# Performance work log

Hardware: AMD Instinct MI355X
Metric: run time of the kernel (lower is better)

Reference implementation:

```python
import jax, jax.numpy as jnp
import numpy as np

N_BLOCKS = 12   # grid rows == cols
D = 256         # per-block feature size (small -> memory-bound)
BATCH = 8192    # samples per block

# Deterministic block-sparse pattern: block (i, j) is active iff (i - j) % 3 == 0.
_mask = np.array([[(i - j) % 3 == 0 for j in range(N_BLOCKS)] for i in range(N_BLOCKS)])
_I, _J = np.nonzero(_mask)  # 48 active blocks
N_ACTIVE = _I.shape[0]


def setup_inputs() -> dict:
    key = jax.random.key(0)
    k1, k2, k3 = jax.random.split(key, 3)
    X = jax.random.normal(k1, (N_BLOCKS, BATCH, D), dtype=jnp.float32)
    # One Linear(D, D) per active block: weight [K, D_in, D_out], bias [K, D_out]
    W = jax.random.normal(k2, (N_ACTIVE, D, D), dtype=jnp.float32) / np.sqrt(D).astype(np.float32)
    b = jax.random.normal(k3, (N_ACTIVE, D), dtype=jnp.float32) * 0.01
    i_idx = jnp.asarray(_I, dtype=jnp.int32)  # output-row index of each active block
    j_idx = jnpim if False else jnp.asarray(_J, dtype=jnp.int32)  # input-col index of each active block
    return {"X": X, "W": W, "b": b, "i_idx": i_idx, "j_idx": j_idx}


def reference(X, W, b, i_idx, j_idx):
    # Gather the input block feeding each active sub-module: [K, BATCH, D]
    Xg = X[j_idx]
    # Apply each block's Linear in one batched contraction: [K, BATCH, D]
    h = jnp.einsum('kbi,kio->kbo', Xg, W) + b[:, None, :]
    # Sum block outputs into their output rows (the '+' combiner / safe_sum):
    # rows with no active block get an all-zero output, matching the zero-vector semantics.
    y = jax.ops.segment_sum(h, i_idx, num_segments=N_BLOCKS)  # [N_BLOCKS, BATCH, D]
    return y
```

## Files before the change

### kernel.cpp

```cpp
#include <hip/hip_runtime.h>

#define N_BLOCKS 12
#define D 256
#define BATCH 8192

typedef __attribute__((ext_vector_type(8))) short bf16x8;
typedef __attribute__((ext_vector_type(4))) float f32x4;

__device__ __forceinline__ unsigned short f2bf(float f) {
  unsigned int u = __float_as_uint(f);
  u += 0x7fffu + ((u >> 16) & 1u);
  return (unsigned short)(u >> 16);
}

__device__ __forceinline__ void gld16(const unsigned short* g, unsigned short* l) {
  __builtin_amdgcn_global_load_lds(
      (const __attribute__((address_space(1))) unsigned int*)g,
      (__attribute__((address_space(3))) unsigned int*)l,
      16, 0, 0);
}

__global__ void cvt_x(const float* __restrict__ X, unsigned short* __restrict__ Xb) {
  const long long t = (long long)blockIdx.x * 256 + threadIdx.x;
  const long long base = t * 8;
  const float4 v0 = *(const float4*)(X + base);
  const float4 v1 = *(const float4*)(X + base + 4);
  uint4 r;
  r.x = (unsigned)f2bf(v0.x) | ((unsigned)f2bf(v0.y) << 16);
  r.y = (unsigned)f2bf(v0.z) | ((unsigned)f2bf(v0.w) << 16);
  r.z = (unsigned)f2bf(v1.x) | ((unsigned)f2bf(v1.y) << 16);
  r.w = (unsigned)f2bf(v1.z) | ((unsigned)f2bf(v1.w) << 16);
  *(uint4*)(Xb + base) = r;
}

__global__ void cvt_w(const float* __restrict__ W, unsigned short* __restrict__ Wt) {
  __shared__ unsigned short tile[32][33];
  const int k  = blockIdx.x >> 6;
  const int t  = blockIdx.x & 63;
  const int ti = t >> 3;
  const int tj = t & 7;
  const float* Wk = W + (long long)k * D * D;
  unsigned short* Wtk = Wt + (long long)k * D * D;
  const int lx = threadIdx.x & 31, ly = threadIdx.x >> 5;
  #pragma unroll
  for (int r = 0; r < 4; ++r) {
    const int i = ti * 32 + ly + r * 8;
    const int o = tj * 32 + lx;
    tile[ly + r * 8][lx] = f2bf(Wk[i * D + o]);
  }
  __syncthreads();
  #pragma unroll
  for (int r = 0; r < 4; ++r) {
    const int o = tj * 32 + ly + r * 8;
    const int i = ti * 32 + lx;
    Wtk[o * D + i] = tile[lx][ly + r * 8];
  }
}

__launch_bounds__(256)
__global__ void bs_gemm(const unsigned short* __restrict__ Xb,
                        const unsigned short* __restrict__ Wt,
                        const float* __restrict__ bias,
                        const int* __restrict__ i_idx,
                        const int* __restrict__ j_idx,
                        int nact,
                        float* __restrict__ Y) {
  __shared__ unsigned short sA[128 * 32];
  __shared__ unsigned short sB[128 * 32];

  const int bid = blockIdx.x;
  const int x   = bid & 7;
  const int r   = bid >> 3;
  const int i   = r >> 4;
  const int rem = r & 15;
  const int bm  = x * 8 + (rem >> 1);
  const int bn  = rem & 1;

  int ks[8], js[8], nk = 0;
  for (int k = 0; k < nact; ++k)
    if (i_idx[k] == i && nk < 8) { ks[nk] = k; js[nk] = j_idx[k]; ++nk; }

  const int tid  = threadIdx.x;
  const int wave = tid >> 6;
  const int lane = tid & 63;
  const int wr   = wave >> 1, wc = wave & 1;

  const int g_off = (tid >> 2) * D + (tid & 3) * 8;
  unsigned short* lA0 = sA + tid * 8;
  unsigned short* lA1 = sA + 2048 + tid * 8;
  unsigned short* lB0 = sB + tid * 8;
  unsigned short* lB1 = sB + 2048 + tid * 8;

  const int q      = lane >> 4;
  const int frag_k = q * 8;
  const int a_row  = wr * 64 + (lane & 15);
  const int b_row  = wc * 64 + (lane & 15);

  f32x4 acc[4][4] = {};

  for (int t = 0; t < nk; ++t) {
    const unsigned short* Ab = Xb + ((long long)js[t] * BATCH + bm * 128) * D + g_off;
    const unsigned short* Bb = Wt + ((long long)ks[t] * D + bn * 128) * D + g_off;
    #pragma unroll
    for (int d0 = 0; d0 < D; d0 += 32) {
      gld16(Ab + d0, lA0);
      gld16(Ab + 64 * D + d0, lA1);
      gld16(Bb + d0, lB0);
      gld16(Bb + 64 * D + d0, lB1);
      __syncthreads();

      bf16x8 aF[4], bF[4];
      #pragma unroll
      for (int mt = 0; mt < 4; ++mt)
        aF[mt] = *(const bf16x8*)(sA + (a_row + mt * 16) * 32 + frag_k);
      #pragma unroll
      for (int nt = 0; nt < 4; ++nt)
        bF[nt] = *(const bf16x8*)(sB + (b_row + nt * 16) * 32 + frag_k);
      #pragma unroll
      for (int mt = 0; mt < 4; ++mt)
        #pragma unroll
        for (int nt = 0; nt < 4; ++nt)
          acc[mt][nt] = __builtin_amdgcn_mfma_f32_16x16x32_bf16(
              aF[mt], bF[nt], acc[mt][nt], 0, 0, 0);
      __syncthreads();
    }
  }

  float* Yb = Y + (long long)i * BATCH * D;
  const int m0 = bm * 128 + wr * 64 + (q * 4);
  const int n0 = bn * 128 + wc * 64 + (lane & 15);
  float bsum[4];
  #pragma unroll
  for (int nt = 0; nt < 4; ++nt) {
    float s = 0.f;
    for (int t = 0; t < nk; ++t) s += bias[ks[t] * D + n0 + nt * 16];
    bsum[nt] = s;
  }
  #pragma unroll
  for (int nt = 0; nt < 4; ++nt) {
    #pragma unroll
    for (int mt = 0; mt < 4; ++mt)
      #pragma unroll
      for (int r2 = 0; r2 < 4; ++r2)
        Yb[(long long)(m0 + mt * 16 + r2) * D + (n0 + nt * 16)] = acc[mt][nt][r2] + bsum[nt];
  }
}

extern "C" void kernel_launch(void* const* d_in, const int* in_sizes, int n_in,
                              void* d_out, int out_size, void* d_ws, size_t ws_size,
                              hipStream_t stream) {
  const float* X = (const float*)d_in[0];
  const float* W = (const float*)d_in[1];
  const float* b = (const float*)d_in[2];
  const int* i_idx = (const int*)d_in[3];
  const int* j_idx = (const int*)d_in[4];
  float* Y = (float*)d_out;
  const int nact = in_sizes[3];

  unsigned short* Xb = (unsigned short*)d_ws;
  unsigned short* Wt = (unsigned short*)((char*)d_ws + (size_t)N_BLOCKS * BATCH * D * 2);

  cvt_x<<<(N_BLOCKS * BATCH * D) / (256 * 8), 256, 0, stream>>>(X, Xb);
  cvt_w<<<nact * 64, 256, 0, stream>>>(W, Wt);
  bs_gemm<<<N_BLOCKS * 64 * 2, 256, 0, stream>>>(Xb, Wt, b, i_idx, j_idx, nact, Y);
}
```

Measured before the change: 261.1 us.

## Triple-buffer LDS pipeline with swizzle and 256x128 tiles in block-sparse GEMM

Restructures the GEMM main loop into a flattened 32-step pipeline across all active blocks, using three LDS stages, prefetching two stages ahead, and a single barrier per step. The tile grows to 256x128 with 512 threads. The LDS layout gets an XOR swizzle to avoid bank conflicts, and blocks are remapped across XCDs for locality. It also caps the number of active blocks per row at 4 with hardcoded registers, which is a correctness risk if more than 4 blocks are active, and it assumes exactly 4 blocks per row by hardcoding 32 steps.

```diff
diff --git a/kernel.cpp b/kernel.cpp
--- a/kernel.cpp
+++ b/kernel.cpp
@@ -57,7 +57,7 @@
   }
 }
 
-__launch_bounds__(256)
+__launch_bounds__(512, 4)
 __global__ void bs_gemm(const unsigned short* __restrict__ Xb,
                         const unsigned short* __restrict__ Wt,
                         const float* __restrict__ bias,
@@ -65,85 +65,130 @@
                         const int* __restrict__ j_idx,
                         int nact,
                         float* __restrict__ Y) {
-  __shared__ unsigned short sA[128 * 32];
-  __shared__ unsigned short sB[128 * 32];
-
-  const int bid = blockIdx.x;
-  const int x   = bid & 7;
-  const int r   = bid >> 3;
-  const int i   = r >> 4;
-  const int rem = r & 15;
-  const int bm  = x * 8 + (rem >> 1);
-  const int bn  = rem & 1;
-
-  int ks[8], js[8], nk = 0;
-  for (int k = 0; k < nact; ++k)
-    if (i_idx[k] == i && nk < 8) { ks[nk] = k; js[nk] = j_idx[k]; ++nk; }
+  __shared__ unsigned short lds[3 * 12288];
+
+  const int bid   = blockIdx.x;
+  const int xcd   = bid & 7;
+  const int local = bid >> 3;
+  const int pp    = local >> 5;
+  const int bm    = local & 31;
+  const int p     = xcd * 3 + pp;
+  const int i     = p >> 1;
+  const int bn    = p & 1;
+
+  int ks0 = 0, ks1 = 0, ks2 = 0, ks3 = 0, js0 = 0, js1 = 0, js2 = 0, js3 = 0, nk = 0;
+  for (int k = 0; k < nact; ++k) {
+    if (i_idx[k] == i) {
+      const int j = j_idx[k];
+      if      (nk == 0) { ks0 = k; js0 = j; }
+      else if (nk == 1) { ks1 = k; js1 = j; }
+      else if (nk == 2) { ks2 = k; js2 = j; }
+      else              { ks3 = k; js3 = j; }
+      ++nk;
+    }
+  }
+#define JS(t) ((t) == 0 ? js0 : (t) == 1 ? js1 : (t) == 2 ? js2 : js3)
+#define KS(t) ((t) == 0 ? ks0 : (t) == 1 ? ks1 : (t) == 2 ? ks2 : ks3)
 
   const int tid  = threadIdx.x;
   const int wave = tid >> 6;
   const int lane = tid & 63;
-  const int wr   = wave >> 1, wc = wave & 1;
-
-  const int g_off = (tid >> 2) * D + (tid & 3) * 8;
-  unsigned short* lA0 = sA + tid * 8;
-  unsigned short* lA1 = sA + 2048 + tid * 8;
-  unsigned short* lB0 = sB + tid * 8;
-  unsigned short* lB1 = sB + 2048 + tid * 8;
-
-  const int q      = lane >> 4;
-  const int frag_k = q * 8;
-  const int a_row  = wr * 64 + (lane & 15);
-  const int b_row  = wc * 64 + (lane & 15);
+  const int wm   = wave >> 1;
+  const int wn   = wave & 1;
+  const int q    = lane >> 4;
+  const int l15  = lane & 15;
+
+  const int srow = tid >> 2;
+  const int sc   = (tid & 3) ^ (srow & 3);
+  const long long sA0 = (long long)srow * D + sc * 8;
+  const long long sA1 = (long long)(srow + 128) * D + sc * 8;
+  const long long sB0 = (long long)srow * D + sc * 8;
+  const int dA0 = tid * 8;
+  const int dA1 = 4096 + tid * 8;
+  const int dB0 = 8192 + tid * 8;
+
+  const int sw  = (q ^ (l15 & 3)) << 4;
+  const int aR0 = (wm * 64 +  0 + l15) * 64 + sw;
+  const int aR1 = (wm * 64 + 16 + l15) * 64 + sw;
+  const int aR2 = (wm * 64 + 32 + l15) * 64 + sw;
+  const int aR3 = (wm * 64 + 48 + l15) * 64 + sw;
+  const int bR0 = 16384 + (wn * 64 +  0 + l15) * 64 + sw;
+  const int bR1 = 16384 + (wn * 64 + 16 + l15) * 64 + sw;
+  const int bR2 = 16384 + (wn * 64 + 32 + l15) * 64 + sw;
+  const int bR3 = 16384 + (wn * 64 + 48 + l15) * 64 + sw;
+
+  auto STAGE = [&](int st) {
+    const int t  = st >> 3;
+    const int kk = st & 7;
+    unsigned short* sl = lds + (st % 3) * 12288;
+    const unsigned short* As =
+        Xb + ((long long)JS(t) * BATCH + bm * 256) * D + kk * 32;
+    const unsigned short* Bs =
+        Wt + ((long long)KS(t) * D + bn * 128) * D + kk * 32;
+    gld16(As + sA0, sl + dA0);
+    gld16(As + sA1, sl + dA1);
+    gld16(Bs + sB0, sl + dB0);
+  };
 
   f32x4 acc[4][4] = {};
 
-  for (int t = 0; t < nk; ++t) {
-    const unsigned short* Ab = Xb + ((long long)js[t] * BATCH + bm * 128) * D + g_off;
-    const unsigned short* Bb = Wt + ((long long)ks[t] * D + bn * 128) * D + g_off;
+  STAGE(0);
+  STAGE(1);
+
+  #pragma unroll
+  for (int kt = 0; kt < 32; ++kt) {
+    if (kt == 31) asm volatile("s_waitcnt vmcnt(0)" ::: "memory");
+    else          asm volatile("s_waitcnt vmcnt(3)" ::: "memory");
+    __builtin_amdgcn_s_barrier();
+    __builtin_amdgcn_sched_barrier(0);
+
+    const char* sb = (const char*)(lds + (kt % 3) * 12288);
+    bf16x8 aF[4], bF[4];
+    aF[0] = *(const bf16x8*)(sb + aR0);
+    aF[1] = *(const bf16x8*)(sb + aR1);
+    aF[2] = *(const bf16x8*)(sb + aR2);
+    aF[3] = *(const bf16x8*)(sb + aR3);
+    bF[0] = *(const bf16x8*)(sb + bR0);
+    bF[1] = *(const bf16x8*)(sb + bR1);
+    bF[2] = *(const bf16x8*)(sb + bR2);
+    bF[3] = *(const bf16x8*)(sb + bR3);
+
+    if (kt < 30) STAGE(kt + 2);
+
+    asm volatile("s_waitcnt lgkmcnt(0)" ::: "memory");
+    __builtin_amdgcn_sched_barrier(0);
+
+    __builtin_amdgcn_s_setprio(1);
     #pragma unroll
-    for (int d0 = 0; d0 < D; d0 += 32) {
-      gld16(Ab + d0, lA0);
-      gld16(Ab + 64 * D + d0, lA1);
-      gld16(Bb + d0, lB0);
-      gld16(Bb + 64 * D + d0, lB1);
-      __syncthreads();
-
-      bf16x8 aF[4], bF[4];
+    for (int mf = 0; mf < 4; ++mf)
       #pragma unroll
-      for (int mt = 0; mt < 4; ++mt)
-        aF[mt] = *(const bf16x8*)(sA + (a_row + mt * 16) * 32 + frag_k);
-      #pragma unroll
-      for (int nt = 0; nt < 4; ++nt)
-        bF[nt] = *(const bf16x8*)(sB + (b_row + nt * 16) * 32 + frag_k);
-      #pragma unroll
-      for (int mt = 0; mt < 4; ++mt)
-        #pragma unroll
-        for (int nt = 0; nt < 4; ++nt)
-          acc[mt][nt] = __builtin_amdgcn_mfma_f32_16x16x32_bf16(
-              aF[mt], bF[nt], acc[mt][nt], 0, 0, 0);
-      __syncthreads();
-    }
+      for (int nf = 0; nf < 4; ++nf)
+        acc[mf][nf] = __builtin_amdgcn_mfma_f32_16x16x32_bf16(
+            aF[mf], bF[nf], acc[mf][nf], 0, 0, 0);
+    __builtin_amdgcn_s_setprio(0);
   }
 
   float* Yb = Y + (long long)i * BATCH * D;
-  const int m0 = bm * 128 + wr * 64 + (q * 4);
-  const int n0 = bn * 128 + wc * 64 + (lane & 15);
+  const int m0 = bm * 256 + wm * 64 + q * 4;
+  const int n0 = bn * 128 + wn * 64 + l15;
   float bsum[4];
   #pragma unroll
-  for (int nt = 0; nt < 4; ++nt) {
+  for (int nf = 0; nf < 4; ++nf) {
     float s = 0.f;
-    for (int t = 0; t < nk; ++t) s += bias[ks[t] * D + n0 + nt * 16];
-    bsum[nt] = s;
-  }
-  #pragma unroll
-  for (int nt = 0; nt < 4; ++nt) {
+    for (int t = 0; t < nk; ++t) s += bias[KS(t) * D + n0 + nf * 16];
+    bsum[nf] = s;
+  }
+  #pragma unroll
+  for (int nf = 0; nf < 4; ++nf) {
     #pragma unroll
-    for (int mt = 0; mt < 4; ++mt)
+    for (int mf = 0; mf < 4; ++mf)
       #pragma unroll
       for (int r2 = 0; r2 < 4; ++r2)
-        Yb[(long long)(m0 + mt * 16 + r2) * D + (n0 + nt * 16)] = acc[mt][nt][r2] + bsum[nt];
-  }
+        Yb[(long long)(m0 + mf * 16 + r2) * D + (n0 + nf * 16)] =
+            acc[mf][nf][r2] + bsum[nf];
+  }
+#undef JS
+#undef KS
 }
 
 extern "C" void kernel_launch(void* const* d_in, const int* in_sizes, int n_in,
@@ -162,5 +207,5 @@
 
   cvt_x<<<(N_BLOCKS * BATCH * D) / (256 * 8), 256, 0, stream>>>(X, Xb);
   cvt_w<<<nact * 64, 256, 0, stream>>>(W, Wt);
-  bs_gemm<<<N_BLOCKS * 64 * 2, 256, 0, stream>>>(Xb, Wt, b, i_idx, j_idx, nact, Y);
-}
+  bs_gemm<<<N_BLOCKS * 32 * 2, 512, 0, stream>>>(Xb, Wt, b, i_idx, j_idx, nact, Y);
+}
```

Result: slower. 276.7 us (+6.0%).
